# Kernel tuning notes

Hardware: AMD Instinct MI355X
Metric: run time of the kernel (lower is better)

## Reference

```python
import jax, jax.numpy as jnp
import numpy as np

B, T, D = 8, 1024, 768
H = 12
DH = D // H
FF = 3072
EPS = 1e-12


def setup_inputs() -> dict:
    key = jax.random.key(0)
    ks = jax.random.split(key, 12)
    s = 0.02
    return {
        "x": jax.random.normal(ks[0], (B, T, D), dtype=jnp.float32),
        "Wq": jax.random.normal(ks[1], (D, D), dtype=jnp.float32) * s,
        "Wk": jax.random.normal(ks[2], (D, D), dtype=jnp.float32) * s,
        "Wv": jax.random.normal(ks[3], (D, D), dtype=jnp.float32) * s,
        "Wo": jax.random.normal(ks[4], (D, D), dtype=jnp.float32) * s,
        "bo": jnp.zeros((D,), dtype=jnp.float32),
        "W1": jax.random.normal(ks[5], (FF, D), dtype=jnp.float32) * s,
        "b1": jnp.zeros((FF,), dtype=jnp.float32),
        "W2": jax.random.normal(ks[6], (D, FF), dtype=jnp.float32) * s,
        "b2": jnp.zeros((D,), dtype=jnp.float32),
        "ln1_w": jnp.ones((D,), dtype=jnp.float32),
        "ln1_b": jnp.zeros((D,), dtype=jnp.float32),
        "ln2_w": jnp.ones((D,), dtype=jnp.float32),
        "ln2_b": jnp.zeros((D,), dtype=jnp.float32),
    }


def _layer_norm(x, w, b, eps=EPS):
    mu = jnp.mean(x, axis=-1, keepdims=True)
    var = jnp.mean((x - mu) ** 2, axis=-1, keepdims=True)
    return (x - mu) * jax.lax.rsqrt(var + eps) * w + b


def _self_attn(x, Wq, Wk, Wv, Wo, bo):
    # x: [B, T, D]; q/k/v projections are bias-free (F.linear with weight only)
    q = (x @ Wq.T).reshape(B, T, H, DH)
    k = (x @ Wk.T).reshape(B, T, H, DH)
    v = (x @ Wv.T).reshape(B, T, H, DH)
    scale = 1.0 / np.sqrt(DH).astype(np.float32)
    scores = jnp.einsum("bqhd,bkhd->bhqk", q, k) * scale  # [B,H,T,T]
    attn = jax.nn.softmax(scores, axis=-1)
    o = jnp.einsum("bhqk,bkhd->bqhd", attn, v).reshape(B, T, D)
    return o @ Wo.T + bo


def reference(x, Wq, Wk, Wv, Wo, bo, W1, b1, W2, b2, ln1_w, ln1_b, ln2_w, ln2_b):
    # Pre-norm ViT encoder block (dropout = 0 / eval mode)
    h = x + _self_attn(_layer_norm(x, ln1_w, ln1_b), Wq, Wk, Wv, Wo, bo)
    z = _layer_norm(h, ln2_w, ln2_b)
    ff = jax.nn.gelu(z @ W1.T + b1, approximate=False) @ W2.T + b2
    return h + ff
```

## Files before the change

### kernel.cpp

```cpp
#include <hip/hip_runtime.h>
#include <hip/hip_bf16.h>
#include <math.h>

#define CB 8
#define CT 1024
#define CD 768
#define CH 12
#define CDH 64
#define CFF 3072
#define CBT 8192

typedef unsigned short u16;
typedef __attribute__((ext_vector_type(8))) short bf16x8;
typedef __attribute__((ext_vector_type(4))) float f32x4;
typedef __attribute__((address_space(1))) unsigned int gu32;
typedef __attribute__((address_space(3))) unsigned int su32;

__device__ __forceinline__ u16 f2bf(float f) {
  union { float f; unsigned u; } v; v.f = f;
  unsigned r = v.u + 0x7fffu + ((v.u >> 16) & 1u);
  return (u16)(r >> 16);
}

__device__ __forceinline__ void gload16(const u16* g, u16* l) {
  __builtin_amdgcn_global_load_lds((gu32*)g, (su32*)l, 16, 0, 0);
}

__device__ __forceinline__ float gelu_f(float x) {
  float y = 0.7978845608028654f * (x + 0.044715f * x * x * x);
  float t = 1.f - 2.f / (__expf(2.f * y) + 1.f);
  return 0.5f * x * (1.f + t);
}

__global__ __launch_bounds__(256) void cvt_bf16(const float* __restrict__ in,
                                                u16* __restrict__ out, int n) {
  int i = blockIdx.x * 256 + threadIdx.x;
  if (i < n) out[i] = f2bf(in[i]);
}

__global__ __launch_bounds__(256) void ln_kernel(const float* __restrict__ X,
                                                 const float* __restrict__ gw,
                                                 const float* __restrict__ gb,
                                                 u16* __restrict__ Y) {
  __shared__ float red[4];
  const int row = blockIdx.x, tid = threadIdx.x;
  const float* xr = X + (size_t)row * CD;
  float v0 = xr[tid], v1 = xr[tid + 256], v2 = xr[tid + 512];
  float s = v0 + v1 + v2;
#pragma unroll
  for (int o = 32; o > 0; o >>= 1) s += __shfl_down(s, o);
  if ((tid & 63) == 0) red[tid >> 6] = s;
  __syncthreads();
  float mu = (red[0] + red[1] + red[2] + red[3]) * (1.f / 768.f);
  __syncthreads();
  float d0 = v0 - mu, d1 = v1 - mu, d2 = v2 - mu;
  float q = d0 * d0 + d1 * d1 + d2 * d2;
#pragma unroll
  for (int o = 32; o > 0; o >>= 1) q += __shfl_down(q, o);
  if ((tid & 63) == 0) red[tid >> 6] = q;
  __syncthreads();
  float var = (red[0] + red[1] + red[2] + red[3]) * (1.f / 768.f);
  float rstd = rsqrtf(var + 1e-12f);
  u16* yr = Y + (size_t)row * CD;
  yr[tid]       = f2bf(d0 * rstd * gw[tid]       + gb[tid]);
  yr[tid + 256] = f2bf(d1 * rstd * gw[tid + 256] + gb[tid + 256]);
  yr[tid + 512] = f2bf(d2 * rstd * gw[tid + 512] + gb[tid + 512]);
}

template <int ACT, int BIAS, int RES, int OMODE>
__global__ __launch_bounds__(256, 4) void gemm_bt(
    const u16* __restrict__ A, const u16* __restrict__ Bt,
    const float* __restrict__ bias, const float* __restrict__ res,
    void* __restrict__ outp, u16* __restrict__ vtp, int M, int N, int K) {
  __shared__ __align__(16) u16 Asm[128 * 64];
  __shared__ __align__(16) u16 Bsm[128 * 64];
  const int tid = threadIdx.x;
  const int gx = gridDim.x;
  const int nwg = gx * gridDim.y;
  const int wg = blockIdx.y * gx + blockIdx.x;
  const int swz = (wg & 7) * (nwg >> 3) + (wg >> 3);
  const int bx = swz % gx, by = swz / gx;
  const int brow = by * 128, bcol = bx * 128;
  const int w = tid >> 6, l = tid & 63;
  const int wm = w >> 1, wn = w & 1;
  const int lr = l & 15, g = l >> 4;
  const f32x4 zf = {0.f, 0.f, 0.f, 0.f};
  f32x4 acc[4][4];
#pragma unroll
  for (int i = 0; i < 4; ++i)
#pragma unroll
    for (int j = 0; j < 4; ++j) acc[i][j] = zf;

  auto stage = [&](int kk) {
#pragma unroll
    for (int rr = 0; rr < 4; ++rr) {
      int c = rr * 256 + tid;
      int row = c >> 3, ch = c & 7;
      int sch = ch ^ (row & 7);
      gload16(A + (size_t)(brow + row) * K + kk + sch * 8, &Asm[(c & ~63) * 8]);
      gload16(Bt + (size_t)(bcol + row) * K + kk + sch * 8, &Bsm[(c & ~63) * 8]);
    }
  };

  const int NT = K >> 6;
  for (int t = 0; t < NT; ++t) {
    stage(t << 6);
    __syncthreads();
    bf16x8 af[4][2], bfr[4][2];
#pragma unroll
    for (int mi = 0; mi < 4; ++mi) {
      const int R = wm * 64 + mi * 16 + lr;
#pragma unroll
      for (int k2 = 0; k2 < 2; ++k2)
        af[mi][k2] = *(const bf16x8*)&Asm[R * 64 + (((k2 * 4 + g) ^ (R & 7)) * 8)];
    }
#pragma unroll
    for (int ni = 0; ni < 4; ++ni) {
      const int R = wn * 64 + ni * 16 + lr;
#pragma unroll
      for (int k2 = 0; k2 < 2; ++k2)
        bfr[ni][k2] = *(const bf16x8*)&Bsm[R * 64 + (((k2 * 4 + g) ^ (R & 7)) * 8)];
    }
#pragma unroll
    for (int k2 = 0; k2 < 2; ++k2)
#pragma unroll
      for (int mi = 0; mi < 4; ++mi)
#pragma unroll
        for (int ni = 0; ni < 4; ++ni)
          acc[mi][ni] = __builtin_amdgcn_mfma_f32_16x16x32_bf16(
              af[mi][k2], bfr[ni][k2], acc[mi][ni], 0, 0, 0);
    __syncthreads();
  }
#pragma unroll
  for (int mi = 0; mi < 4; ++mi) {
#pragma unroll
    for (int ni = 0; ni < 4; ++ni) {
      const int col = bcol + wn * 64 + ni * 16 + lr;
      float bv = 0.f;
      if (BIAS) bv = bias[col];
#pragma unroll
      for (int r = 0; r < 4; ++r) {
        const int row = brow + wm * 64 + mi * 16 + g * 4 + r;
        float v = acc[mi][ni][r] + bv;
        if (ACT == 1) v = gelu_f(v);
        if (RES) v += res[(size_t)row * N + col];
        if (OMODE == 0) {
          ((float*)outp)[(size_t)row * N + col] = v;
        } else if (OMODE == 1) {
          ((u16*)outp)[(size_t)row * N + col] = f2bf(v);
        } else {
          if (bcol < 2 * CD) {
            ((u16*)outp)[(size_t)row * (2 * CD) + col] = f2bf(v);
          } else {
            int vc = col - 2 * CD;
            int hI = vc >> 6, dI = vc & 63;
            int bI = row >> 10, tI = row & 1023;
            vtp[((size_t)((bI * CH + hI) * 64 + dI)) * CT + tI] = f2bf(v);
          }
        }
      }
    }
  }
}

__global__ __launch_bounds__(256) void attn_fa(const u16* __restrict__ QK,
                                               const u16* __restrict__ Vt,
                                               u16* __restrict__ O) {
  __shared__ __align__(16) u16 Ksm[2][64 * 64];
  __shared__ __align__(16) u16 Vsm[2][64 * 64];
  __shared__ __align__(16) u16 Psm[4 * 32 * 64];
  const int LDQ = 2 * CD;
  const int tid = threadIdx.x;
  const int w = tid >> 6, l = tid & 63;
  const int lr = l & 15, g = l >> 4;
  const int wg = (blockIdx.z * CH + blockIdx.y) * 8 + blockIdx.x;
  const int swzid = (wg & 7) * 96 + (wg >> 3);
  const int qb = (swzid & 7) * 128;
  const int rem = swzid >> 3;
  const int hh = rem % CH;
  const int bb = rem / CH;
  const size_t rowb = (size_t)bb * CT;
  const int hc = hh * CDH;
  const u16* Qp = QK;
  const u16* Kp = QK + CD;
  const size_t vbase = (size_t)((bb * CH + hh) * 64) * CT;

  bf16x8 qA0, qA1, qB0, qB1;
  {
    const u16* qr = Qp + (rowb + qb + w * 32 + lr) * LDQ + hc;
    qA0 = *(const bf16x8*)(qr + g * 8);
    qA1 = *(const bf16x8*)(qr + 32 + g * 8);
    const u16* qr2 = qr + 16 * LDQ;
    qB0 = *(const bf16x8*)(qr2 + g * 8);
    qB1 = *(const bf16x8*)(qr2 + 32 + g * 8);
  }
  const f32x4 zf = {0.f, 0.f, 0.f, 0.f};
  f32x4 oA[4], oB[4];
#pragma unroll
  for (int i = 0; i < 4; ++i) { oA[i] = zf; oB[i] = zf; }
  float lsA[4] = {0.f, 0.f, 0.f, 0.f};
  float lsB[4] = {0.f, 0.f, 0.f, 0.f};
  u16* Pw = Psm + w * (32 * 64);

  auto stage = [&](int buf, int kt) {
#pragma unroll
    for (int rr = 0; rr < 2; ++rr) {
      int c = rr * 256 + tid;
      int trow = c >> 3, tch = c & 7;
      int sch = tch ^ (trow & 7);
      gload16(Kp + (rowb + kt + trow) * LDQ + hc + sch * 8, &Ksm[buf][(c & ~63) * 8]);
      gload16(Vt + vbase + (size_t)trow * CT + kt + sch * 8, &Vsm[buf][(c & ~63) * 8]);
    }
  };

  stage(0, 0);
  __syncthreads();
  for (int t = 0; t < CT / 64; ++t) {
    const int cur = t & 1;
    if (t + 1 < CT / 64) stage(cur ^ 1, (t + 1) * 64);
#pragma unroll
    for (int ni = 0; ni < 4; ++ni) {
      const int krow = (ni * 16 + lr) * 64;
      bf16x8 kf0 = *(const bf16x8*)&Ksm[cur][krow + ((g ^ (lr & 7)) * 8)];
      bf16x8 kf1 = *(const bf16x8*)&Ksm[cur][krow + (((4 + g) ^ (lr & 7)) * 8)];
      f32x4 zA = zf, zB = zf;
      zA = __builtin_amdgcn_mfma_f32_16x16x32_bf16(qA0, kf0, zA, 0, 0, 0);
      zA = __builtin_amdgcn_mfma_f32_16x16x32_bf16(qA1, kf1, zA, 0, 0, 0);
      zB = __builtin_amdgcn_mfma_f32_16x16x32_bf16(qB0, kf0, zB, 0, 0, 0);
      zB = __builtin_amdgcn_mfma_f32_16x16x32_bf16(qB1, kf1, zB, 0, 0, 0);
      const int pcol = ni * 2 + (lr >> 3);
#pragma unroll
      for (int r = 0; r < 4; ++r) {
        const int prow = g * 4 + r;
        float pA = __expf(zA[r] * 0.125f);
        float pB = __expf(zB[r] * 0.125f);
        lsA[r] += pA;
        lsB[r] += pB;
        const int sw = ((pcol ^ (prow & 7)) << 3) + (lr & 7);
        Pw[prow * 64 + sw] = f2bf(pA);
        Pw[(prow + 16) * 64 + sw] = f2bf(pB);
      }
    }
#pragma unroll
    for (int ks = 0; ks < 2; ++ks) {
      const int pch = (((ks * 4 + g) ^ (lr & 7)) << 3);
      bf16x8 pfA = *(const bf16x8*)&Pw[lr * 64 + pch];
      bf16x8 pfB = *(const bf16x8*)&Pw[(16 + lr) * 64 + pch];
#pragma unroll
      for (int ni = 0; ni < 4; ++ni) {
        bf16x8 vf = *(const bf16x8*)&Vsm[cur][(ni * 16 + lr) * 64 + pch];
        oA[ni] = __builtin_amdgcn_mfma_f32_16x16x32_bf16(pfA, vf, oA[ni], 0, 0, 0);
        oB[ni] = __builtin_amdgcn_mfma_f32_16x16x32_bf16(pfB, vf, oB[ni], 0, 0, 0);
      }
    }
    __syncthreads();
  }
#pragma unroll
  for (int o = 8; o > 0; o >>= 1)
#pragma unroll
    for (int r = 0; r < 4; ++r) {
      lsA[r] += __shfl_xor(lsA[r], o);
      lsB[r] += __shfl_xor(lsB[r], o);
    }
  float invA[4], invB[4];
#pragma unroll
  for (int r = 0; r < 4; ++r) {
    invA[r] = 1.f / lsA[r];
    invB[r] = 1.f / lsB[r];
  }
#pragma unroll
  for (int ni = 0; ni < 4; ++ni)
#pragma unroll
    for (int r = 0; r < 4; ++r) {
      const size_t rA = rowb + qb + w * 32 + g * 4 + r;
      O[rA * CD + hc + ni * 16 + lr] = f2bf(oA[ni][r] * invA[r]);
      O[(rA + 16) * CD + hc + ni * 16 + lr] = f2bf(oB[ni][r] * invB[r]);
    }
}

extern "C" void kernel_launch(void* const* d_in, const int* in_sizes, int n_in,
                              void* d_out, int out_size, void* d_ws, size_t ws_size,
                              hipStream_t stream) {
  (void)in_sizes; (void)n_in; (void)out_size; (void)ws_size;
  const float* x    = (const float*)d_in[0];
  const float* Wq   = (const float*)d_in[1];
  const float* Wk   = (const float*)d_in[2];
  const float* Wv   = (const float*)d_in[3];
  const float* Wo   = (const float*)d_in[4];
  const float* bo   = (const float*)d_in[5];
  const float* W1   = (const float*)d_in[6];
  const float* b1   = (const float*)d_in[7];
  const float* W2   = (const float*)d_in[8];
  const float* b2   = (const float*)d_in[9];
  const float* ln1w = (const float*)d_in[10];
  const float* ln1b = (const float*)d_in[11];
  const float* ln2w = (const float*)d_in[12];
  const float* ln2b = (const float*)d_in[13];
  float* out = (float*)d_out;

  char* ws = (char*)d_ws;
  size_t off = 0;
  auto alloc = [&](size_t bytes) -> char* {
    char* p = ws + off;
    off += (bytes + 255) & ~(size_t)255;
    return p;
  };
  u16* wqkv = (u16*)alloc((size_t)3 * CD * CD * 2);
  u16* wob  = (u16*)alloc((size_t)CD * CD * 2);
  u16* w1b  = (u16*)alloc((size_t)CFF * CD * 2);
  u16* w2b  = (u16*)alloc((size_t)CD * CFF * 2);
  u16* xn   = (u16*)alloc((size_t)CBT * CD * 2);
  u16* qk   = (u16*)alloc((size_t)CBT * 2 * CD * 2);
  u16* vt   = (u16*)alloc((size_t)CBT * CD * 2);
  float* hb = (float*)alloc((size_t)CBT * CD * 4);
  u16* ff1  = (u16*)alloc((size_t)CBT * CFF * 2);

  u16* attnb = xn;
  u16* zb = qk;

  const int DD = CD * CD;
  const int DF = CD * CFF;
  cvt_bf16<<<dim3((DD + 255) / 256), dim3(256), 0, stream>>>(Wq, wqkv, DD);
  cvt_bf16<<<dim3((DD + 255) / 256), dim3(256), 0, stream>>>(Wk, wqkv + DD, DD);
  cvt_bf16<<<dim3((DD + 255) / 256), dim3(256), 0, stream>>>(Wv, wqkv + 2 * DD, DD);
  cvt_bf16<<<dim3((DD + 255) / 256), dim3(256), 0, stream>>>(Wo, wob, DD);
  cvt_bf16<<<dim3((DF + 255) / 256), dim3(256), 0, stream>>>(W1, w1b, DF);
  cvt_bf16<<<dim3((DF + 255) / 256), dim3(256), 0, stream>>>(W2, w2b, DF);

  ln_kernel<<<dim3(CBT), dim3(256), 0, stream>>>(x, ln1w, ln1b, xn);

  gemm_bt<0, 0, 0, 2><<<dim3(3 * CD / 128, CBT / 128), dim3(256), 0, stream>>>(
      xn, wqkv, nullptr, nullptr, qk, vt, CBT, 3 * CD, CD);

  attn_fa<<<dim3(CT / 128, CH, CB), dim3(256), 0, stream>>>(qk, vt, attnb);

  gemm_bt<0, 1, 1, 0><<<dim3(CD / 128, CBT / 128), dim3(256), 0, stream>>>(
      attnb, wob, bo, x, hb, nullptr, CBT, CD, CD);

  ln_kernel<<<dim3(CBT), dim3(256), 0, stream>>>(hb, ln2w, ln2b, zb);

  gemm_bt<1, 1, 0, 1><<<dim3(CFF / 128, CBT / 128), dim3(256), 0, stream>>>(
      zb, w1b, b1, nullptr, ff1, nullptr, CBT, CFF, CD);

  gemm_bt<0, 1, 1, 0><<<dim3(CD / 128, CBT / 128), dim3(256), 0, stream>>>(
      ff1, w2b, b2, hb, out, nullptr, CBT, CD, CFF);
}
```

Before: 266.5 us.

## Add 256x256-tile pipelined GEMM for QKV and FFN1 projections

Adds a new 512-thread GEMM kernel with 256x256 output tiles, double-buffered LDS with XOR swizzle, staged half-tile async loads interleaved with MFMA phases, workgroup swizzling, and setprio around MFMA blocks. The QKV projection and the FFN up-projection (with GELU) now use it instead of the 128x128 kernel. The aim is more data reuse per tile and better overlap of global loads with compute. The trade-off is fewer workgroups (e.g. 9x32 for QKV), which may underfill the GPU's compute units, plus higher register and LDS pressure.

```diff
diff --git a/kernel.cpp b/kernel.cpp
--- a/kernel.cpp
+++ b/kernel.cpp
@@ -147,6 +147,134 @@
         if (OMODE == 0) {
           ((float*)outp)[(size_t)row * N + col] = v;
         } else if (OMODE == 1) {
+          ((u16*)outp)[(size_t)row * N + col] = f2bf(v);
+        } else {
+          if (bcol < 2 * CD) {
+            ((u16*)outp)[(size_t)row * (2 * CD) + col] = f2bf(v);
+          } else {
+            int vc = col - 2 * CD;
+            int hI = vc >> 6, dI = vc & 63;
+            int bI = row >> 10, tI = row & 1023;
+            vtp[((size_t)((bI * CH + hI) * 64 + dI)) * CT + tI] = f2bf(v);
+          }
+        }
+      }
+    }
+  }
+}
+
+template <int ACT, int BIAS, int OMODE>
+__global__ __launch_bounds__(512, 2) void gemm256(
+    const u16* __restrict__ A, const u16* __restrict__ Bt,
+    const float* __restrict__ bias,
+    void* __restrict__ outp, u16* __restrict__ vtp, int M, int N, int K) {
+  __shared__ __align__(16) u16 SM[2][2][256 * 64];
+  const int tid = threadIdx.x;
+  const int gx = gridDim.x;
+  const int nwg = gx * gridDim.y;
+  const int wg = blockIdx.y * gx + blockIdx.x;
+  const int swz = (wg & 7) * (nwg >> 3) + (wg >> 3);
+  const int bx = swz % gx, by = swz / gx;
+  const int brow = by * 256, bcol = bx * 256;
+  const int w = tid >> 6, l = tid & 63;
+  const int wm = w & 1, wn = w >> 1;
+  const int lr = l & 15, g = l >> 4;
+  const f32x4 zf = {0.f, 0.f, 0.f, 0.f};
+  f32x4 acc[8][4];
+#pragma unroll
+  for (int i = 0; i < 8; ++i)
+#pragma unroll
+    for (int j = 0; j < 4; ++j) acc[i][j] = zf;
+
+  auto stageH = [&](int mat, int half, int buf, int kk) {
+    const u16* P = mat ? Bt : A;
+    const int gbase = (mat ? bcol : brow) + half * 128;
+    u16* dst = &SM[mat][buf][half * (128 * 64)];
+#pragma unroll
+    for (int r2 = 0; r2 < 2; ++r2) {
+      int c = r2 * 512 + tid;
+      int row = c >> 3, ch = c & 7;
+      int sch = ch ^ (row & 7);
+      gload16(P + (size_t)(gbase + row) * K + kk + sch * 8, dst + (c & ~63) * 8);
+    }
+  };
+
+  const int NT = K >> 6;
+  stageH(1, 0, 0, 0);
+  stageH(1, 1, 0, 0);
+  stageH(0, 0, 0, 0);
+  stageH(0, 1, 0, 0);
+  stageH(1, 0, 1, 64);
+  stageH(1, 1, 1, 64);
+  stageH(0, 0, 1, 64);
+  asm volatile("s_waitcnt vmcnt(6)" ::: "memory");
+  __builtin_amdgcn_s_barrier();
+
+  for (int U = 0; U < NT; ++U) {
+    const int cur = U & 1;
+    const u16* Ac = &SM[0][cur][0];
+    const u16* Bc = &SM[1][cur][0];
+    bf16x8 bfr[4][2];
+#pragma unroll
+    for (int p = 0; p < 4; ++p) {
+      bf16x8 af[2][2];
+#pragma unroll
+      for (int m2 = 0; m2 < 2; ++m2) {
+        const int ar = (p * 2 + m2) * 32 + wm * 16 + lr;
+#pragma unroll
+        for (int ks = 0; ks < 2; ++ks)
+          af[m2][ks] = *(const bf16x8*)&Ac[ar * 64 + (((ks * 4 + g) ^ (ar & 7)) << 3)];
+      }
+      if (p == 0) {
+#pragma unroll
+        for (int ni = 0; ni < 4; ++ni) {
+          const int br = wn * 64 + ni * 16 + lr;
+#pragma unroll
+          for (int ks = 0; ks < 2; ++ks)
+            bfr[ni][ks] = *(const bf16x8*)&Bc[br * 64 + (((ks * 4 + g) ^ (br & 7)) << 3)];
+        }
+      }
+      if (p == 0) {
+        if (U + 1 < NT) stageH(0, 1, cur ^ 1, (U + 1) << 6);
+      } else if (U + 2 < NT) {
+        if (p == 1)      stageH(1, 0, cur, (U + 2) << 6);
+        else if (p == 2) stageH(1, 1, cur, (U + 2) << 6);
+        else             stageH(0, 0, cur, (U + 2) << 6);
+      }
+      __builtin_amdgcn_s_barrier();
+      asm volatile("s_waitcnt lgkmcnt(0)" ::: "memory");
+      __builtin_amdgcn_sched_barrier(0);
+      __builtin_amdgcn_s_setprio(1);
+#pragma unroll
+      for (int ks = 0; ks < 2; ++ks)
+#pragma unroll
+        for (int m2 = 0; m2 < 2; ++m2)
+#pragma unroll
+          for (int ni = 0; ni < 4; ++ni)
+            acc[p * 2 + m2][ni] = __builtin_amdgcn_mfma_f32_16x16x32_bf16(
+                af[m2][ks], bfr[ni][ks], acc[p * 2 + m2][ni], 0, 0, 0);
+      __builtin_amdgcn_s_setprio(0);
+      if (p == 3 && U + 1 < NT) {
+        if (U + 1 == NT - 1) asm volatile("s_waitcnt vmcnt(0)" ::: "memory");
+        else                 asm volatile("s_waitcnt vmcnt(6)" ::: "memory");
+      }
+      __builtin_amdgcn_s_barrier();
+    }
+  }
+
+#pragma unroll
+  for (int mi = 0; mi < 8; ++mi) {
+#pragma unroll
+    for (int ni = 0; ni < 4; ++ni) {
+      const int col = bcol + wn * 64 + ni * 16 + lr;
+      float bv = 0.f;
+      if (BIAS) bv = bias[col];
+#pragma unroll
+      for (int r = 0; r < 4; ++r) {
+        const int row = brow + mi * 32 + wm * 16 + g * 4 + r;
+        float v = acc[mi][ni][r] + bv;
+        if (ACT == 1) v = gelu_f(v);
+        if (OMODE == 1) {
           ((u16*)outp)[(size_t)row * N + col] = f2bf(v);
         } else {
           if (bcol < 2 * CD) {
@@ -329,8 +457,8 @@
 
   ln_kernel<<<dim3(CBT), dim3(256), 0, stream>>>(x, ln1w, ln1b, xn);
 
-  gemm_bt<0, 0, 0, 2><<<dim3(3 * CD / 128, CBT / 128), dim3(256), 0, stream>>>(
-      xn, wqkv, nullptr, nullptr, qk, vt, CBT, 3 * CD, CD);
+  gemm256<0, 0, 2><<<dim3(3 * CD / 256, CBT / 256), dim3(512), 0, stream>>>(
+      xn, wqkv, nullptr, qk, vt, CBT, 3 * CD, CD);
 
   attn_fa<<<dim3(CT / 128, CH, CB), dim3(256), 0, stream>>>(qk, vt, attnb);
 
@@ -339,8 +467,8 @@
 
   ln_kernel<<<dim3(CBT), dim3(256), 0, stream>>>(hb, ln2w, ln2b, zb);
 
-  gemm_bt<1, 1, 0, 1><<<dim3(CFF / 128, CBT / 128), dim3(256), 0, stream>>>(
-      zb, w1b, b1, nullptr, ff1, nullptr, CBT, CFF, CD);
+  gemm256<1, 1, 1><<<dim3(CFF / 256, CBT / 256), dim3(512), 0, stream>>>(
+      zb, w1b, b1, ff1, nullptr, CBT, CFF, CD);
 
   gemm_bt<0, 1, 1, 0><<<dim3(CD / 128, CBT / 128), dim3(256), 0, stream>>>(
       ff1, w2b, b2, hb, out, nullptr, CBT, CD, CFF);
```

Result: slower. 310.9 us (+16.7%).
